# Optimization experiments

Hardware: AMD Instinct MI355X
Metric: run time of the kernel (lower is better)

Reference implementation:

```python
import jax, jax.numpy as jnp
import numpy as np

NUM_AGENTS = 8
D_AGENT = 64  # input_dim_single_agent
INPUT_DIM = NUM_AGENTS * D_AGENT
NORM_TERM = NUM_AGENTS - 1 if NUM_AGENTS > 1 else 1
BATCH = 65536


def setup_inputs() -> dict:
    key = jax.random.key(0)
    k1, k2, k3 = jax.random.split(key, 3)
    x = jax.random.normal(k1, (BATCH, INPUT_DIM), dtype=jnp.float32)
    # original code multiplies hidden_weights by 0.1 (twice-written bug leaves comm unscaled)
    hidden_weights = jax.random.normal(k2, (D_AGENT, D_AGENT), dtype=jnp.float32) * 0.1
    communication_weights = jax.random.normal(k3, (D_AGENT, D_AGENT), dtype=jnp.float32)
    return {"x": x, "hidden_weights": hidden_weights,
            "communication_weights": communication_weights}


def reference(x, hidden_weights, communication_weights):
    # Equivalent to y = tanh(x @ final_mat.T) where final_mat has diagonal
    # [d,d] blocks = hidden_weights and off-diagonal blocks = comm/(A-1).
    B = x.shape[0]
    xb = x.reshape(B, NUM_AGENTS, D_AGENT)          # [B, A, d]
    others = xb.sum(axis=1, keepdims=True) - xb      # sum over other agents
    # F.linear uses weight W with out = x @ W.T, hence 'ed' contraction on d
    y = (jnp.einsum('bad,ed->bae', xb, hidden_weights)
         + jnp.einsum('bad,ed->bae', others, communication_weights) / NORM_TERM)
    return jnp.tanh(y).reshape(B, INPUT_DIM)
```

## Files before the change

kernel.cpp:

```cpp
#include <hip/hip_runtime.h>


typedef _Float16 half4v __attribute__((ext_vector_type(4)));
typedef _Float16 half8v __attribute__((ext_vector_type(8)));
typedef float    floatx4 __attribute__((ext_vector_type(4)));

#define TILE_ROWS 16
#define M_TILE    128
#define LDS_STRIDE 136
#define TILES_PER_BLOCK 2

__global__ __launch_bounds__(256, 3)
void comm_kernel(const float* __restrict__ x,
                 const float* __restrict__ Hw,
                 const float* __restrict__ Cw,
                 float* __restrict__ out)
{
    __shared__ __align__(16) _Float16 aug[M_TILE * LDS_STRIDE];

    const int tid  = threadIdx.x;
    const int lane = tid & 63;
    const int wave = tid >> 6;
    const int quad = lane >> 4;
    const int l16  = lane & 15;

    #pragma unroll
    for (int i = 0; i < 8; ++i) {
        const int fh = (i * 256 + tid) * 4;
        const int e = fh >> 7;
        const int k = fh & 127;
        half4v hv;
        if (k < 64) {
            const float4 h = *reinterpret_cast<const float4*>(Hw + e * 64 + k);
            const float4 c = *reinterpret_cast<const float4*>(Cw + e * 64 + k);
            hv[0] = (_Float16)(h.x - c.x * (1.0f / 7.0f));
            hv[1] = (_Float16)(h.y - c.y * (1.0f / 7.0f));
            hv[2] = (_Float16)(h.z - c.z * (1.0f / 7.0f));
            hv[3] = (_Float16)(h.w - c.w * (1.0f / 7.0f));
        } else {
            const float4 c = *reinterpret_cast<const float4*>(Cw + e * 64 + (k - 64));
            hv[0] = (_Float16)(c.x * (1.0f / 7.0f));
            hv[1] = (_Float16)(c.y * (1.0f / 7.0f));
            hv[2] = (_Float16)(c.z * (1.0f / 7.0f));
            hv[3] = (_Float16)(c.w * (1.0f / 7.0f));
        }
        *reinterpret_cast<half4v*>(&aug[e * LDS_STRIDE + k]) = hv;
    }
    __syncthreads();

    half8v bfrag[4][4];
    #pragma unroll
    for (int kt = 0; kt < 4; ++kt)
        #pragma unroll
        for (int nt = 0; nt < 4; ++nt)
            bfrag[kt][nt] = *reinterpret_cast<const half8v*>(
                &aug[(nt * 16 + l16) * LDS_STRIDE + kt * 32 + quad * 8]);
    __syncthreads();

    #pragma unroll 1
    for (int t = 0; t < TILES_PER_BLOCK; ++t) {
        const int  tile = blockIdx.x * TILES_PER_BLOCK + t;
        const long row0 = (long)tile * TILE_ROWS;
        const float* xt = x + row0 * 512;

        if (t) __syncthreads();

        #pragma unroll
        for (int i = 0; i < 8; ++i) {
            const int flat = (tid + i * 256) * 4;
            const float4 v = *reinterpret_cast<const float4*>(xt + flat);
            const int r   = flat >> 9;
            const int c   = flat & 511;
            const int row = (r << 3) + (c >> 6);
            const int k   = c & 63;
            half4v hv;
            hv[0] = (_Float16)v.x; hv[1] = (_Float16)v.y;
            hv[2] = (_Float16)v.z; hv[3] = (_Float16)v.w;
            *reinterpret_cast<half4v*>(&aug[row * LDS_STRIDE + k]) = hv;
        }
        __syncthreads();

        {
            const int r  = tid >> 4;
            const int d0 = (tid & 15) << 2;
            float s0 = 0.f, s1 = 0.f, s2 = 0.f, s3 = 0.f;
            #pragma unroll
            for (int a = 0; a < 8; ++a) {
                const half4v p = *reinterpret_cast<const half4v*>(
                    &aug[(r * 8 + a) * LDS_STRIDE + d0]);
                s0 += (float)p[0]; s1 += (float)p[1];
                s2 += (float)p[2]; s3 += (float)p[3];
            }
            half4v sv;
            sv[0] = (_Float16)s0; sv[1] = (_Float16)s1;
            sv[2] = (_Float16)s2; sv[3] = (_Float16)s3;
            #pragma unroll
            for (int a = 0; a < 8; ++a)
                *reinterpret_cast<half4v*>(
                    &aug[(r * 8 + a) * LDS_STRIDE + 64 + d0]) = sv;
        }
        __syncthreads();

        floatx4 acc[2][4];
        #pragma unroll
        for (int mt = 0; mt < 2; ++mt)
            #pragma unroll
            for (int nt = 0; nt < 4; ++nt)
                acc[mt][nt] = floatx4{0.f, 0.f, 0.f, 0.f};

        #pragma unroll
        for (int mt = 0; mt < 2; ++mt) {
            const int mrow = wave * 32 + mt * 16 + l16;
            #pragma unroll
            for (int kt = 0; kt < 4; ++kt) {
                const half8v af = *reinterpret_cast<const half8v*>(
                    &aug[mrow * LDS_STRIDE + kt * 32 + quad * 8]);
                #pragma unroll
                for (int nt = 0; nt < 4; ++nt)
                    acc[mt][nt] = __builtin_amdgcn_mfma_f32_16x16x32_f16(
                        af, bfrag[kt][nt], acc[mt][nt], 0, 0, 0);
            }
        }

        float* o = out + (long)tile * (M_TILE * 64);
        #pragma unroll
        for (int mt = 0; mt < 2; ++mt) {
            const int mbase = wave * 32 + mt * 16 + quad * 4;
            #pragma unroll
            for (int nt = 0; nt < 4; ++nt) {
                const int e = nt * 16 + l16;
                #pragma unroll
                for (int reg = 0; reg < 4; ++reg) {
                    float y = acc[mt][nt][reg];
                    y = fminf(10.f, fmaxf(-10.f, y));
                    const float tv = __builtin_amdgcn_exp2f(y * 2.8853900817779268f);
                    const float res = (tv - 1.f) * __builtin_amdgcn_rcpf(tv + 1.f);
                    o[(mbase + reg) * 64 + e] = res;
                }
            }
        }
    }
}

extern "C" void kernel_launch(void* const* d_in, const int* in_sizes, int n_in,
                              void* d_out, int out_size, void* d_ws, size_t ws_size,
                              hipStream_t stream) {
    const float* x  = (const float*)d_in[0];
    const float* Hw = (const float*)d_in[1];
    const float* Cw = (const float*)d_in[2];
    float* out = (float*)d_out;

    const int rows   = in_sizes[0] / 512;
    const int blocks = rows / (TILE_ROWS * TILES_PER_BLOCK);
    comm_kernel<<<blocks, 256, 0, stream>>>(x, Hw, Cw, out);
}
```

Measured before the change: 247.8 us.

## Drop LDS staging; load x fragments directly into MFMA layout with shuffle reduction

Removes the shared-memory tile and all block barriers. Each wave now loads its 16-row-by-64 x tile straight from global memory into MFMA A-fragment registers, and computes the sum over agents with cross-lane xor shuffles instead of an LDS reduction. Weight fragments are built directly from global memory per lane, and a persistent grid-stride loop over 1024 blocks replaces the fixed one-block-per-pair-of-tiles launch. Global loads become strided 32-byte chunks per lane rather than fully coalesced float4 rows, and the shuffles add VALU and cross-lane work.

```diff
diff --git a/kernel.cpp b/kernel.cpp
--- a/kernel.cpp
+++ b/kernel.cpp
@@ -1,142 +1,102 @@
 #include <hip/hip_runtime.h>
 
 
-typedef _Float16 half4v __attribute__((ext_vector_type(4)));
-typedef _Float16 half8v __attribute__((ext_vector_type(8)));
+typedef _Float16 half8v  __attribute__((ext_vector_type(8)));
 typedef float    floatx4 __attribute__((ext_vector_type(4)));
 
-#define TILE_ROWS 16
-#define M_TILE    128
-#define LDS_STRIDE 136
-#define TILES_PER_BLOCK 2
+#define WAVES_PER_BLOCK 4
 
-__global__ __launch_bounds__(256, 3)
+__global__ __launch_bounds__(256, 4)
 void comm_kernel(const float* __restrict__ x,
                  const float* __restrict__ Hw,
                  const float* __restrict__ Cw,
-                 float* __restrict__ out)
+                 float* __restrict__ out,
+                 int ntiles, int nwaves)
 {
-    __shared__ __align__(16) _Float16 aug[M_TILE * LDS_STRIDE];
-
     const int tid  = threadIdx.x;
     const int lane = tid & 63;
     const int wave = tid >> 6;
     const int quad = lane >> 4;
     const int l16  = lane & 15;
-
-    #pragma unroll
-    for (int i = 0; i < 8; ++i) {
-        const int fh = (i * 256 + tid) * 4;
-        const int e = fh >> 7;
-        const int k = fh & 127;
-        half4v hv;
-        if (k < 64) {
-            const float4 h = *reinterpret_cast<const float4*>(Hw + e * 64 + k);
-            const float4 c = *reinterpret_cast<const float4*>(Cw + e * 64 + k);
-            hv[0] = (_Float16)(h.x - c.x * (1.0f / 7.0f));
-            hv[1] = (_Float16)(h.y - c.y * (1.0f / 7.0f));
-            hv[2] = (_Float16)(h.z - c.z * (1.0f / 7.0f));
-            hv[3] = (_Float16)(h.w - c.w * (1.0f / 7.0f));
-        } else {
-            const float4 c = *reinterpret_cast<const float4*>(Cw + e * 64 + (k - 64));
-            hv[0] = (_Float16)(c.x * (1.0f / 7.0f));
-            hv[1] = (_Float16)(c.y * (1.0f / 7.0f));
-            hv[2] = (_Float16)(c.z * (1.0f / 7.0f));
-            hv[3] = (_Float16)(c.w * (1.0f / 7.0f));
-        }
-        *reinterpret_cast<half4v*>(&aug[e * LDS_STRIDE + k]) = hv;
-    }
-    __syncthreads();
+    const int wgid = blockIdx.x * WAVES_PER_BLOCK + wave;
 
     half8v bfrag[4][4];
     #pragma unroll
-    for (int kt = 0; kt < 4; ++kt)
+    for (int nt = 0; nt < 4; ++nt) {
+        const float* hr = Hw + (nt * 16 + l16) * 64 + quad * 8;
+        const float* cr = Cw + (nt * 16 + l16) * 64 + quad * 8;
+        float h[16], c[16];
+        *reinterpret_cast<float4*>(&h[0])  = *reinterpret_cast<const float4*>(hr);
+        *reinterpret_cast<float4*>(&h[4])  = *reinterpret_cast<const float4*>(hr + 4);
+        *reinterpret_cast<float4*>(&h[8])  = *reinterpret_cast<const float4*>(hr + 32);
+        *reinterpret_cast<float4*>(&h[12]) = *reinterpret_cast<const float4*>(hr + 36);
+        *reinterpret_cast<float4*>(&c[0])  = *reinterpret_cast<const float4*>(cr);
+        *reinterpret_cast<float4*>(&c[4])  = *reinterpret_cast<const float4*>(cr + 4);
+        *reinterpret_cast<float4*>(&c[8])  = *reinterpret_cast<const float4*>(cr + 32);
+        *reinterpret_cast<float4*>(&c[12]) = *reinterpret_cast<const float4*>(cr + 36);
+        half8v b0, b1, b2, b3;
         #pragma unroll
-        for (int nt = 0; nt < 4; ++nt)
-            bfrag[kt][nt] = *reinterpret_cast<const half8v*>(
-                &aug[(nt * 16 + l16) * LDS_STRIDE + kt * 32 + quad * 8]);
-    __syncthreads();
+        for (int j = 0; j < 8; ++j) {
+            b0[j] = (_Float16)(h[j]     - c[j]     * (1.0f / 7.0f));
+            b1[j] = (_Float16)(h[8 + j] - c[8 + j] * (1.0f / 7.0f));
+            b2[j] = (_Float16)(c[j]     * (1.0f / 7.0f));
+            b3[j] = (_Float16)(c[8 + j] * (1.0f / 7.0f));
+        }
+        bfrag[0][nt] = b0; bfrag[1][nt] = b1;
+        bfrag[2][nt] = b2; bfrag[3][nt] = b3;
+    }
 
-    #pragma unroll 1
-    for (int t = 0; t < TILES_PER_BLOCK; ++t) {
-        const int  tile = blockIdx.x * TILES_PER_BLOCK + t;
-        const long row0 = (long)tile * TILE_ROWS;
-        const float* xt = x + row0 * 512;
+    for (int t = wgid; t < ntiles; t += nwaves) {
+        const float* xt = x + (size_t)t * 1024 + l16 * 64 + quad * 8;
+        float xf[16];
+        *reinterpret_cast<float4*>(&xf[0])  = *reinterpret_cast<const float4*>(xt);
+        *reinterpret_cast<float4*>(&xf[4])  = *reinterpret_cast<const float4*>(xt + 4);
+        *reinterpret_cast<float4*>(&xf[8])  = *reinterpret_cast<const float4*>(xt + 32);
+        *reinterpret_cast<float4*>(&xf[12]) = *reinterpret_cast<const float4*>(xt + 36);
 
-        if (t) __syncthreads();
+        half8v af0, af1;
+        #pragma unroll
+        for (int j = 0; j < 8; ++j) {
+            af0[j] = (_Float16)xf[j];
+            af1[j] = (_Float16)xf[8 + j];
+        }
 
         #pragma unroll
-        for (int i = 0; i < 8; ++i) {
-            const int flat = (tid + i * 256) * 4;
-            const float4 v = *reinterpret_cast<const float4*>(xt + flat);
-            const int r   = flat >> 9;
-            const int c   = flat & 511;
-            const int row = (r << 3) + (c >> 6);
-            const int k   = c & 63;
-            half4v hv;
-            hv[0] = (_Float16)v.x; hv[1] = (_Float16)v.y;
-            hv[2] = (_Float16)v.z; hv[3] = (_Float16)v.w;
-            *reinterpret_cast<half4v*>(&aug[row * LDS_STRIDE + k]) = hv;
+        for (int m = 1; m <= 4; m <<= 1) {
+            #pragma unroll
+            for (int j = 0; j < 16; ++j)
+                xf[j] += __shfl_xor(xf[j], m, 64);
         }
-        __syncthreads();
+        half8v af2, af3;
+        #pragma unroll
+        for (int j = 0; j < 8; ++j) {
+            af2[j] = (_Float16)xf[j];
+            af3[j] = (_Float16)xf[8 + j];
+        }
 
-        {
-            const int r  = tid >> 4;
-            const int d0 = (tid & 15) << 2;
-            float s0 = 0.f, s1 = 0.f, s2 = 0.f, s3 = 0.f;
-            #pragma unroll
-            for (int a = 0; a < 8; ++a) {
-                const half4v p = *reinterpret_cast<const half4v*>(
-                    &aug[(r * 8 + a) * LDS_STRIDE + d0]);
-                s0 += (float)p[0]; s1 += (float)p[1];
-                s2 += (float)p[2]; s3 += (float)p[3];
-            }
-            half4v sv;
-            sv[0] = (_Float16)s0; sv[1] = (_Float16)s1;
-            sv[2] = (_Float16)s2; sv[3] = (_Float16)s3;
-            #pragma unroll
-            for (int a = 0; a < 8; ++a)
-                *reinterpret_cast<half4v*>(
-                    &aug[(r * 8 + a) * LDS_STRIDE + 64 + d0]) = sv;
-        }
-        __syncthreads();
-
-        floatx4 acc[2][4];
+        floatx4 acc[4];
         #pragma unroll
-        for (int mt = 0; mt < 2; ++mt)
-            #pragma unroll
-            for (int nt = 0; nt < 4; ++nt)
-                acc[mt][nt] = floatx4{0.f, 0.f, 0.f, 0.f};
+        for (int nt = 0; nt < 4; ++nt) acc[nt] = floatx4{0.f, 0.f, 0.f, 0.f};
 
         #pragma unroll
-        for (int mt = 0; mt < 2; ++mt) {
-            const int mrow = wave * 32 + mt * 16 + l16;
-            #pragma unroll
-            for (int kt = 0; kt < 4; ++kt) {
-                const half8v af = *reinterpret_cast<const half8v*>(
-                    &aug[mrow * LDS_STRIDE + kt * 32 + quad * 8]);
-                #pragma unroll
-                for (int nt = 0; nt < 4; ++nt)
-                    acc[mt][nt] = __builtin_amdgcn_mfma_f32_16x16x32_f16(
-                        af, bfrag[kt][nt], acc[mt][nt], 0, 0, 0);
-            }
+        for (int nt = 0; nt < 4; ++nt) {
+            acc[nt] = __builtin_amdgcn_mfma_f32_16x16x32_f16(af0, bfrag[0][nt], acc[nt], 0, 0, 0);
+            acc[nt] = __builtin_amdgcn_mfma_f32_16x16x32_f16(af1, bfrag[1][nt], acc[nt], 0, 0, 0);
+            acc[nt] = __builtin_amdgcn_mfma_f32_16x16x32_f16(af2, bfrag[2][nt], acc[nt], 0, 0, 0);
+            acc[nt] = __builtin_amdgcn_mfma_f32_16x16x32_f16(af3, bfrag[3][nt], acc[nt], 0, 0, 0);
         }
 
-        float* o = out + (long)tile * (M_TILE * 64);
+        float* o = out + (size_t)t * 1024;
         #pragma unroll
-        for (int mt = 0; mt < 2; ++mt) {
-            const int mbase = wave * 32 + mt * 16 + quad * 4;
+        for (int nt = 0; nt < 4; ++nt) {
+            const int e = nt * 16 + l16;
             #pragma unroll
-            for (int nt = 0; nt < 4; ++nt) {
-                const int e = nt * 16 + l16;
-                #pragma unroll
-                for (int reg = 0; reg < 4; ++reg) {
-                    float y = acc[mt][nt][reg];
-                    y = fminf(10.f, fmaxf(-10.f, y));
-                    const float tv = __builtin_amdgcn_exp2f(y * 2.8853900817779268f);
-                    const float res = (tv - 1.f) * __builtin_amdgcn_rcpf(tv + 1.f);
-                    o[(mbase + reg) * 64 + e] = res;
-                }
+            for (int reg = 0; reg < 4; ++reg) {
+                float y = acc[nt][reg];
+                y = fminf(10.f, fmaxf(-10.f, y));
+                const float tv  = __builtin_amdgcn_exp2f(y * 2.8853900817779268f);
+                const float res = (tv - 1.f) * __builtin_amdgcn_rcpf(tv + 1.f);
+                o[(quad * 4 + reg) * 64 + e] = res;
             }
         }
     }
@@ -151,6 +111,8 @@
     float* out = (float*)d_out;
 
     const int rows   = in_sizes[0] / 512;
-    const int blocks = rows / (TILE_ROWS * TILES_PER_BLOCK);
-    comm_kernel<<<blocks, 256, 0, stream>>>(x, Hw, Cw, out);
+    const int ntiles = rows * 8 / 16;
+    const int blocks = 1024;
+    const int nwaves = blocks * WAVES_PER_BLOCK;
+    comm_kernel<<<blocks, 256, 0, stream>>>(x, Hw, Cw, out, ntiles, nwaves);
 }
```

Result: no change. 249.1 us (+0.5%).
